# Kernel optimization log

Measured on AMD Instinct MI355X. Metric: run time of the kernel, lower is better.

Reference implementation:

```python
import jax, jax.numpy as jnp
import numpy as np

N = 100_000      # nodes
E = 1_600_000    # edges
F_IN = 256       # num_node_features
H = 128          # hidden_dim
G = 1_000        # graphs in batch


def setup_inputs() -> dict:
    key = jax.random.key(0)
    ks = jax.random.split(key, 12)
    x = jax.random.normal(ks[0], (N, F_IN), jnp.float32)
    edge_index = jax.random.randint(ks[1], (2, E), 0, N)
    batch = jnp.sort(jax.random.randint(ks[2], (N,), 0, G))
    def w(k, shape):
        fan_in = shape[0]
        return jax.random.normal(k, shape, jnp.float32) / np.sqrt(fan_in)
    return {
        "x": x,
        "edge_index": edge_index,
        "batch": batch,
        "W1": w(ks[3], (F_IN, H)), "b1": jnp.zeros((H,), jnp.float32),
        "W2": w(ks[4], (H, H)),    "b2": jnp.zeros((H,), jnp.float32),
        "W3": w(ks[5], (H, H)),    "b3": jnp.zeros((H,), jnp.float32),
        "fw1": w(ks[6], (H, 32)),  "fb1": jnp.zeros((32,), jnp.float32),
        "fw2": w(ks[7], (32, 2)),  "fb2": jnp.zeros((2,), jnp.float32),
    }


def reference(x, edge_index, batch, W1, b1, W2, b2, W3, b3, fw1, fb1, fw2, fb2):
    # GCN normalization with self-loops (PyG GCNConv defaults)
    loop = jnp.arange(N)
    src = jnp.concatenate([edge_index[0], loop])  # [E+N]
    dst = jnp.concatenate([edge_index[1], loop])
    deg = jax.ops.segment_sum(jnp.ones(E + N, x.dtype), dst, num_segments=N)
    dis = jnp.where(deg > 0, jax.lax.rsqrt(deg), 0.0)
    norm = (dis[src] * dis[dst])[:, None]  # [E+N, 1]

    def gcn(h, W, b):
        h = h @ W                                    # linear transform first (fewer bytes moved)
        msg = h[src] * norm                          # gather + scale
        return jax.ops.segment_sum(msg, dst, num_segments=N) + b  # scatter-add

    h = jax.nn.relu(gcn(x, W1, b1))   # dropout = identity (eval mode)
    h = jax.nn.relu(gcn(h, W2, b2))
    h = jax.nn.relu(gcn(h, W3, b3))

    # global_mean_pool over graph ids
    sums = jax.ops.segment_sum(h, batch, num_segments=G)          # [G, H]
    cnt = jax.ops.segment_sum(jnp.ones(N, h.dtype), batch, num_segments=G)
    g = sums / jnp.maximum(cnt, 1.0)[:, None]

    g = jax.nn.relu(g @ fw1 + fb1)
    logits = g @ fw2 + fb2
    return jax.nn.log_softmax(logits, axis=1)
```

## Files before the change

### kernel.cpp

```cpp
#include <hip/hip_runtime.h>
#include <hip/hip_bf16.h>
#include <math.h>

#define N_NODES 100000
#define N_EDGES 1600000
#define F_IN 256
#define H_DIM 128
#define N_GRAPHS 1000

#define NB_BUCKETS ((N_NODES + 255) >> 8)
#define BSTRIDE 392
#define A_BLOCKS 256
#define EPB (N_EDGES / A_BLOCKS)

typedef unsigned short bfu;
typedef unsigned char u8;
typedef short short8 __attribute__((ext_vector_type(8)));
typedef float f32x4 __attribute__((ext_vector_type(4)));
typedef float f32x2 __attribute__((ext_vector_type(2)));

__device__ __forceinline__ float b2f(unsigned u) {
    union { unsigned int i; float f; } v;
    v.i = u << 16;
    return v.f;
}
__device__ __forceinline__ bfu f2b(float f) {
    __hip_bfloat16 h = __float2bfloat16(f);
    return *reinterpret_cast<bfu*>(&h);
}
__device__ __forceinline__ unsigned pk4_fp8(float v0, float v1, float v2, float v3) {
    int r = __builtin_amdgcn_cvt_pk_fp8_f32(v0, v1, 0, false);
    r = __builtin_amdgcn_cvt_pk_fp8_f32(v2, v3, r, true);
    return (unsigned)r;
}
__device__ __forceinline__ void acc4_fp8(float* a, unsigned v) {
    f32x2 p;
    p = __builtin_amdgcn_cvt_pk_f32_fp8((int)v, false); a[0] += p.x; a[1] += p.y;
    p = __builtin_amdgcn_cvt_pk_f32_fp8((int)v, true);  a[2] += p.x; a[3] += p.y;
}
__device__ __forceinline__ void acc16_fp8(float* a, uint4 v) {
    acc4_fp8(a, v.x); acc4_fp8(a + 4, v.y); acc4_fp8(a + 8, v.z); acc4_fp8(a + 12, v.w);
}

__global__ __launch_bounds__(256) void k_hist(const int* __restrict__ dst,
                                              int* __restrict__ cnt_bb) {
    __shared__ int h[BSTRIDE];
    const int t = threadIdx.x;
    for (int i = t; i < BSTRIDE; i += 256) h[i] = 0;
    __syncthreads();
    const int base = blockIdx.x * EPB;
    for (int i = t; i < EPB; i += 256) atomicAdd(&h[dst[base + i] >> 8], 1);
    __syncthreads();
    for (int i = t; i < NB_BUCKETS; i += 256) cnt_bb[blockIdx.x * BSTRIDE + i] = h[i];
}

__global__ __launch_bounds__(256) void k_scan_blocks(int* __restrict__ cnt_bb,
                                                     int* __restrict__ btot) {
    __shared__ int s[256];
    const int t = threadIdx.x;
    const int b = blockIdx.x;
    int v = cnt_bb[t * BSTRIDE + b];
    s[t] = v;
    __syncthreads();
    for (int off = 1; off < 256; off <<= 1) {
        int u = (t >= off) ? s[t - off] : 0;
        __syncthreads();
        s[t] += u;
        __syncthreads();
    }
    cnt_bb[t * BSTRIDE + b] = s[t] - v;
    if (t == 255) btot[b] = s[255];
}

__global__ __launch_bounds__(512) void k_scan_buckets(const int* __restrict__ btot,
                                                      int* __restrict__ bucket_base) {
    __shared__ int s[512];
    const int t = threadIdx.x;
    int v = (t < NB_BUCKETS) ? btot[t] : 0;
    s[t] = v;
    __syncthreads();
    for (int off = 1; off < 512; off <<= 1) {
        int u = (t >= off) ? s[t - off] : 0;
        __syncthreads();
        s[t] += u;
        __syncthreads();
    }
    if (t < NB_BUCKETS) bucket_base[t] = s[t] - v;
    if (t == 0) bucket_base[NB_BUCKETS] = N_EDGES;
}

__global__ __launch_bounds__(256) void k_stage(const int* __restrict__ src,
                                               const int* __restrict__ dst,
                                               const int* __restrict__ cnt_bb,
                                               const int* __restrict__ bucket_base,
                                               unsigned* __restrict__ staging) {
    __shared__ int cur[BSTRIDE];
    const int t = threadIdx.x;
    const int blk = blockIdx.x;
    for (int i = t; i < NB_BUCKETS; i += 256)
        cur[i] = bucket_base[i] + cnt_bb[blk * BSTRIDE + i];
    __syncthreads();
    const int base = blk * EPB;
    for (int i = t; i < EPB; i += 256) {
        int d = dst[base + i];
        int s = src[base + i];
        int b = d >> 8;
        int pos = atomicAdd(&cur[b], 1);
        staging[pos] = (unsigned)s | ((unsigned)(d & 255) << 24);
    }
}

__global__ __launch_bounds__(256) void k_bucket(const unsigned* __restrict__ staging,
                                                const int* __restrict__ bucket_base,
                                                int* __restrict__ row_ptr,
                                                float* __restrict__ dis,
                                                int* __restrict__ col) {
    __shared__ int h[256];
    __shared__ int sc[256];
    __shared__ int cur[256];
    const int t = threadIdx.x;
    const int b = blockIdx.x;
    const int s0 = bucket_base[b];
    const int ne = bucket_base[b + 1] - s0;
    h[t] = 0;
    __syncthreads();
    for (int i = t; i < ne; i += 256) atomicAdd(&h[staging[s0 + i] >> 24], 1);
    __syncthreads();
    int myc = h[t];
    sc[t] = myc;
    __syncthreads();
    for (int off = 1; off < 256; off <<= 1) {
        int u = (t >= off) ? sc[t - off] : 0;
        __syncthreads();
        sc[t] += u;
        __syncthreads();
    }
    int excl = sc[t] - myc;
    int node = b * 256 + t;
    if (node <= N_NODES) row_ptr[node] = s0 + excl;
    if (node < N_NODES) dis[node] = rsqrtf((float)(myc + 1));
    cur[t] = s0 + excl;
    __syncthreads();
    for (int i = t; i < ne; i += 256) {
        unsigned u = staging[s0 + i];
        int pos = atomicAdd(&cur[u >> 24], 1);
        col[pos] = (int)(u & 0xFFFFFFu);
    }
}

__device__ __forceinline__ void wpack_one(const float* __restrict__ W,
                                          bfu* __restrict__ Wp, int u) {
    int lane = u & 63;
    int nf = (u >> 6) & 7;
    int ks = u >> 9;
    int k = ks * 32 + (lane >> 4) * 8;
    int n = nf * 16 + (lane & 15);
    bfu o[8];
#pragma unroll
    for (int j = 0; j < 8; ++j) o[j] = f2b(W[(k + j) * 128 + n]);
    uint4 pk;
    pk.x = (unsigned)o[0] | ((unsigned)o[1] << 16);
    pk.y = (unsigned)o[2] | ((unsigned)o[3] << 16);
    pk.z = (unsigned)o[4] | ((unsigned)o[5] << 16);
    pk.w = (unsigned)o[6] | ((unsigned)o[7] << 16);
    *(uint4*)&Wp[u * 8] = pk;
}

__global__ __launch_bounds__(256) void k_misc(const float* __restrict__ W1,
                                              const float* __restrict__ W2,
                                              const float* __restrict__ W3,
                                              bfu* __restrict__ wp1, bfu* __restrict__ wp2,
                                              bfu* __restrict__ wp3,
                                              const int* __restrict__ batch,
                                              int* __restrict__ bounds) {
    const int b = blockIdx.x, t = threadIdx.x;
    if (b < 16) {
        wpack_one(W1, wp1, b * 256 + t);
    } else if (b < 24) {
        wpack_one(W2, wp2, (b - 16) * 256 + t);
    } else if (b < 32) {
        wpack_one(W3, wp3, (b - 24) * 256 + t);
    } else {
        int g = (b - 32) * 256 + t;
        if (g <= N_GRAPHS) {
            int lo = 0, hi = N_NODES;
            while (lo < hi) {
                int mid = (lo + hi) >> 1;
                if (batch[mid] < g) lo = mid + 1; else hi = mid;
            }
            bounds[g] = lo;
        }
    }
}

__global__ __launch_bounds__(256, 4) void k_mm1(const float* __restrict__ A,
                                                const bfu* __restrict__ Wp,
                                                const float* __restrict__ dis,
                                                u8* __restrict__ C8, int M) {
    const int t = threadIdx.x;
    const int w = t >> 6, l = t & 63, l15 = l & 15, lhi = l >> 4;
    const int row = blockIdx.x * 64 + w * 16 + l15;
    const int rowc = row < M ? row : M - 1;
    const float* ap = A + (long)rowc * 256 + lhi * 8;

    float4 va[8][2];
#pragma unroll
    for (int ks = 0; ks < 8; ++ks) {
        va[ks][0] = *(const float4*)(ap + ks * 32);
        va[ks][1] = *(const float4*)(ap + ks * 32 + 4);
    }

    f32x4 acc[8];
#pragma unroll
    for (int nf = 0; nf < 8; ++nf) acc[nf] = (f32x4)0.0f;

#pragma unroll
    for (int ks = 0; ks < 8; ++ks) {
        unsigned p0 = (unsigned)f2b(va[ks][0].x) | ((unsigned)f2b(va[ks][0].y) << 16);
        unsigned p1 = (unsigned)f2b(va[ks][0].z) | ((unsigned)f2b(va[ks][0].w) << 16);
        unsigned p2 = (unsigned)f2b(va[ks][1].x) | ((unsigned)f2b(va[ks][1].y) << 16);
        unsigned p3 = (unsigned)f2b(va[ks][1].z) | ((unsigned)f2b(va[ks][1].w) << 16);
        uint4 afu = make_uint4(p0, p1, p2, p3);
        short8 af = *(short8*)&afu;
        const bfu* wp = Wp + ((long)(ks * 8) * 64 + l) * 8;
#pragma unroll
        for (int nf = 0; nf < 8; ++nf) {
            short8 wf = *(const short8*)(wp + (long)nf * 64 * 8);
            acc[nf] = __builtin_amdgcn_mfma_f32_16x16x32_bf16(wf, af, acc[nf], 0, 0, 0);
        }
    }
    if (row < M) {
        float sc = dis[row];
        int nb0 = lhi * 4;
#pragma unroll
        for (int nf = 0; nf < 8; ++nf) {
            unsigned pk = pk4_fp8(acc[nf][0] * sc, acc[nf][1] * sc,
                                  acc[nf][2] * sc, acc[nf][3] * sc);
            *(unsigned*)&C8[(long)row * 128 + nf * 16 + nb0] = pk;
        }
    }
}

__global__ __launch_bounds__(256) void k_agg_mm(const int* __restrict__ row_ptr,
                                                const int* __restrict__ col,
                                                const float* __restrict__ dis,
                                                const u8* __restrict__ tprev8,
                                                const float* __restrict__ bvec,
                                                const bfu* __restrict__ Wp,
                                                u8* __restrict__ tnext8, int M) {
    __shared__ bfu Hs[64 * 136];
    const int t = threadIdx.x;
    const int nrow = t >> 2;
    const int node = blockIdx.x * 64 + nrow;
    const int lz = t & 3;
    const int ch = lz * 32;

    if (node < M) {
        float a[32];
#pragma unroll
        for (int j = 0; j < 32; ++j) a[j] = 0.0f;
        const u8* tp = tprev8 + ch;
        {
            const u8* r = tp + (long)node * 128;
            acc16_fp8(a, *(const uint4*)r);
            acc16_fp8(a + 16, *(const uint4*)(r + 16));
        }
        int e = row_ptr[node];
        const int end = row_ptr[node + 1];
        for (; e + 1 < end; e += 2) {
            int s0 = col[e], s1 = col[e + 1];
            const u8* r0 = tp + (long)s0 * 128;
            const u8* r1 = tp + (long)s1 * 128;
            uint4 v00 = *(const uint4*)r0;
            uint4 v01 = *(const uint4*)(r0 + 16);
            uint4 v10 = *(const uint4*)r1;
            uint4 v11 = *(const uint4*)(r1 + 16);
            acc16_fp8(a, v00); acc16_fp8(a + 16, v01);
            acc16_fp8(a, v10); acc16_fp8(a + 16, v11);
        }
        if (e < end) {
            const u8* r = tp + (long)col[e] * 128;
            acc16_fp8(a, *(const uint4*)r);
            acc16_fp8(a + 16, *(const uint4*)(r + 16));
        }
        const float dn = dis[node];
        uint pk[16];
#pragma unroll
        for (int j = 0; j < 16; ++j) {
            float lo = fmaxf(a[2 * j] * dn + bvec[ch + 2 * j], 0.0f);
            float hi = fmaxf(a[2 * j + 1] * dn + bvec[ch + 2 * j + 1], 0.0f);
            pk[j] = (unsigned)f2b(lo) | ((unsigned)f2b(hi) << 16);
        }
        bfu* hrow = &Hs[nrow * 136 + ch];
#pragma unroll
        for (int q = 0; q < 4; ++q)
            *(uint4*)(hrow + q * 8) = make_uint4(pk[4 * q], pk[4 * q + 1], pk[4 * q + 2], pk[4 * q + 3]);
    }
    __syncthreads();
    const int w = t >> 6, l = t & 63, l15 = l & 15, lhi = l >> 4;
    f32x4 acc[8];
#pragma unroll
    for (int nf = 0; nf < 8; ++nf) acc[nf] = (f32x4)0.0f;
#pragma unroll
    for (int ks = 0; ks < 4; ++ks) {
        short8 af = *(const short8*)&Hs[(w * 16 + l15) * 136 + ks * 32 + lhi * 8];
        const bfu* wp = Wp + ((long)(ks * 8) * 64 + l) * 8;
#pragma unroll
        for (int nf = 0; nf < 8; ++nf) {
            short8 wf = *(const short8*)(wp + (long)nf * 64 * 8);
            acc[nf] = __builtin_amdgcn_mfma_f32_16x16x32_bf16(wf, af, acc[nf], 0, 0, 0);
        }
    }
    int row = blockIdx.x * 64 + w * 16 + l15;
    if (row < M) {
        float sc = dis[row];
        int nb0 = lhi * 4;
#pragma unroll
        for (int nf = 0; nf < 8; ++nf) {
            unsigned pko = pk4_fp8(acc[nf][0] * sc, acc[nf][1] * sc,
                                   acc[nf][2] * sc, acc[nf][3] * sc);
            *(unsigned*)&tnext8[(long)row * 128 + nf * 16 + nb0] = pko;
        }
    }
}

__global__ __launch_bounds__(256) void k_agg8(const int* __restrict__ row_ptr,
                                              const int* __restrict__ col,
                                              const float* __restrict__ dis,
                                              const u8* __restrict__ t8,
                                              const float* __restrict__ b,
                                              bfu* __restrict__ h) {
    const int t = threadIdx.x;
    const int node = blockIdx.x * 8 + (t >> 5);
    const int lane = t & 31;
    if (node >= N_NODES) return;
    const int q = lane << 2;

    const u8* tp = t8 + q;
    float a[4] = {0.f, 0.f, 0.f, 0.f};
    acc4_fp8(a, *(const unsigned*)&tp[(long)node * 128]);

    int e = row_ptr[node];
    const int end = row_ptr[node + 1];
    for (; e + 3 < end; e += 4) {
        int s0 = col[e], s1 = col[e + 1], s2 = col[e + 2], s3 = col[e + 3];
        unsigned v0 = *(const unsigned*)&tp[(long)s0 * 128];
        unsigned v1 = *(const unsigned*)&tp[(long)s1 * 128];
        unsigned v2 = *(const unsigned*)&tp[(long)s2 * 128];
        unsigned v3 = *(const unsigned*)&tp[(long)s3 * 128];
        acc4_fp8(a, v0); acc4_fp8(a, v1); acc4_fp8(a, v2); acc4_fp8(a, v3);
    }
    for (; e < end; ++e)
        acc4_fp8(a, *(const unsigned*)&tp[(long)col[e] * 128]);

    const float dn = dis[node];
    float4 bb = *(const float4*)&b[q];
    float o0 = fmaxf(a[0] * dn + bb.x, 0.0f);
    float o1 = fmaxf(a[1] * dn + bb.y, 0.0f);
    float o2 = fmaxf(a[2] * dn + bb.z, 0.0f);
    float o3 = fmaxf(a[3] * dn + bb.w, 0.0f);
    uint2 pk;
    pk.x = (unsigned)f2b(o0) | ((unsigned)f2b(o1) << 16);
    pk.y = (unsigned)f2b(o2) | ((unsigned)f2b(o3) << 16);
    *(uint2*)&h[(long)node * 128 + q] = pk;
}

__global__ __launch_bounds__(128) void k_pool_head(const int* __restrict__ bounds,
                                                   const bfu* __restrict__ h,
                                                   const float* __restrict__ fw1, const float* __restrict__ fb1,
                                                   const float* __restrict__ fw2, const float* __restrict__ fb2,
                                                   float* __restrict__ out) {
    const int g = blockIdx.x;
    const int t = threadIdx.x;
    const int s = bounds[g], e = bounds[g + 1];
    float sum = 0.0f;
    int n = s;
    for (; n + 1 < e; n += 2) {
        sum += b2f(h[(long)n * 128 + t]);
        sum += b2f(h[(long)(n + 1) * 128 + t]);
    }
    if (n < e) sum += b2f(h[(long)n * 128 + t]);

    __shared__ float sg[128];
    __shared__ float sh[32];
    float inv = 1.0f / fmaxf((float)(e - s), 1.0f);
    sg[t] = sum * inv;
    __syncthreads();
    if (t < 32) {
        float a = fb1[t];
#pragma unroll 8
        for (int k = 0; k < 128; ++k) a += sg[k] * fw1[k * 32 + t];
        sh[t] = fmaxf(a, 0.0f);
    }
    __syncthreads();
    if (t == 0) {
        float l0 = fb2[0], l1 = fb2[1];
        for (int k = 0; k < 32; ++k) {
            l0 += sh[k] * fw2[k * 2];
            l1 += sh[k] * fw2[k * 2 + 1];
        }
        float m = fmaxf(l0, l1);
        float lse = m + logf(expf(l0 - m) + expf(l1 - m));
        out[g * 2 + 0] = l0 - lse;
        out[g * 2 + 1] = l1 - lse;
    }
}

extern "C" void kernel_launch(void* const* d_in, const int* in_sizes, int n_in,
                              void* d_out, int out_size, void* d_ws, size_t ws_size,
                              hipStream_t stream) {
    const float* x  = (const float*)d_in[0];
    const int* ei   = (const int*)d_in[1];
    const int* batch = (const int*)d_in[2];
    const float* W1 = (const float*)d_in[3];
    const float* b1 = (const float*)d_in[4];
    const float* W2 = (const float*)d_in[5];
    const float* b2 = (const float*)d_in[6];
    const float* W3 = (const float*)d_in[7];
    const float* b3 = (const float*)d_in[8];
    const float* fw1 = (const float*)d_in[9];
    const float* fb1 = (const float*)d_in[10];
    const float* fw2 = (const float*)d_in[11];
    const float* fb2 = (const float*)d_in[12];
    float* out = (float*)d_out;

    const int* src = ei;
    const int* dst = ei + N_EDGES;

    char* ws = (char*)d_ws;
    int*      cnt_bb      = (int*)ws;
    int*      btot        = cnt_bb + A_BLOCKS * BSTRIDE;
    int*      bucket_base = btot + BSTRIDE;
    unsigned* staging     = (unsigned*)(bucket_base + BSTRIDE + 8);
    int*      row_ptr     = (int*)(staging + N_EDGES);
    float*    dis         = (float*)(row_ptr + N_NODES + 4);
    int*      col         = (int*)(dis + N_NODES);
    int*      bounds      = col + N_EDGES;
    bfu*      wpack1      = (bfu*)(bounds + N_GRAPHS + 8);
    bfu*      wpack2      = wpack1 + 32768;
    bfu*      wpack3      = wpack2 + 16384;
    u8*       bufA8       = (u8*)(wpack3 + 16384);
    u8*       bufB8       = bufA8 + (long)N_NODES * 128;
    u8*       bufC8       = bufB8 + (long)N_NODES * 128;
    bfu*      bufD        = (bfu*)(bufC8 + (long)N_NODES * 128);

    k_hist<<<A_BLOCKS, 256, 0, stream>>>(dst, cnt_bb);
    k_scan_blocks<<<NB_BUCKETS, 256, 0, stream>>>(cnt_bb, btot);
    k_scan_buckets<<<1, 512, 0, stream>>>(btot, bucket_base);
    k_stage<<<A_BLOCKS, 256, 0, stream>>>(src, dst, cnt_bb, bucket_base, staging);
    k_bucket<<<NB_BUCKETS, 256, 0, stream>>>(staging, bucket_base, row_ptr, dis, col);
    k_misc<<<36, 256, 0, stream>>>(W1, W2, W3, wpack1, wpack2, wpack3, batch, bounds);

    const int mm1Grid = (N_NODES + 63) / 64;
    const int fusedGrid = (N_NODES + 63) / 64;
    const int aggGrid = (N_NODES + 7) / 8;

    k_mm1<<<mm1Grid, 256, 0, stream>>>(x, wpack1, dis, bufA8, N_NODES);
    k_agg_mm<<<fusedGrid, 256, 0, stream>>>(row_ptr, col, dis, bufA8, b1, wpack2, bufB8, N_NODES);
    k_agg_mm<<<fusedGrid, 256, 0, stream>>>(row_ptr, col, dis, bufB8, b2, wpack3, bufC8, N_NODES);
    k_agg8<<<aggGrid, 256, 0, stream>>>(row_ptr, col, dis, bufC8, b3, bufD);

    k_pool_head<<<N_GRAPHS, 128, 0, stream>>>(bounds, bufD, fw1, fb1, fw2, fb2, out);
}
```

Baseline: 310.2 us.

## Unfuse aggregation and matmul into separate agg8 and mm2 kernels

```diff
diff --git a/kernel.cpp b/kernel.cpp
--- a/kernel.cpp
+++ b/kernel.cpp
@@ -37,9 +37,6 @@
     f32x2 p;
     p = __builtin_amdgcn_cvt_pk_f32_fp8((int)v, false); a[0] += p.x; a[1] += p.y;
     p = __builtin_amdgcn_cvt_pk_f32_fp8((int)v, true);  a[2] += p.x; a[3] += p.y;
-}
-__device__ __forceinline__ void acc16_fp8(float* a, uint4 v) {
-    acc4_fp8(a, v.x); acc4_fp8(a + 4, v.y); acc4_fp8(a + 8, v.z); acc4_fp8(a + 12, v.w);
 }
 
 __global__ __launch_bounds__(256) void k_hist(const int* __restrict__ dst,
@@ -241,89 +238,6 @@
     }
 }
 
-__global__ __launch_bounds__(256) void k_agg_mm(const int* __restrict__ row_ptr,
-                                                const int* __restrict__ col,
-                                                const float* __restrict__ dis,
-                                                const u8* __restrict__ tprev8,
-                                                const float* __restrict__ bvec,
-                                                const bfu* __restrict__ Wp,
-                                                u8* __restrict__ tnext8, int M) {
-    __shared__ bfu Hs[64 * 136];
-    const int t = threadIdx.x;
-    const int nrow = t >> 2;
-    const int node = blockIdx.x * 64 + nrow;
-    const int lz = t & 3;
-    const int ch = lz * 32;
-
-    if (node < M) {
-        float a[32];
-#pragma unroll
-        for (int j = 0; j < 32; ++j) a[j] = 0.0f;
-        const u8* tp = tprev8 + ch;
-        {
-            const u8* r = tp + (long)node * 128;
-            acc16_fp8(a, *(const uint4*)r);
-            acc16_fp8(a + 16, *(const uint4*)(r + 16));
-        }
-        int e = row_ptr[node];
-        const int end = row_ptr[node + 1];
-        for (; e + 1 < end; e += 2) {
-            int s0 = col[e], s1 = col[e + 1];
-            const u8* r0 = tp + (long)s0 * 128;
-            const u8* r1 = tp + (long)s1 * 128;
-            uint4 v00 = *(const uint4*)r0;
-            uint4 v01 = *(const uint4*)(r0 + 16);
-            uint4 v10 = *(const uint4*)r1;
-            uint4 v11 = *(const uint4*)(r1 + 16);
-            acc16_fp8(a, v00); acc16_fp8(a + 16, v01);
-            acc16_fp8(a, v10); acc16_fp8(a + 16, v11);
-        }
-        if (e < end) {
-            const u8* r = tp + (long)col[e] * 128;
-            acc16_fp8(a, *(const uint4*)r);
-            acc16_fp8(a + 16, *(const uint4*)(r + 16));
-        }
-        const float dn = dis[node];
-        uint pk[16];
-#pragma unroll
-        for (int j = 0; j < 16; ++j) {
-            float lo = fmaxf(a[2 * j] * dn + bvec[ch + 2 * j], 0.0f);
-            float hi = fmaxf(a[2 * j + 1] * dn + bvec[ch + 2 * j + 1], 0.0f);
-            pk[j] = (unsigned)f2b(lo) | ((unsigned)f2b(hi) << 16);
-        }
-        bfu* hrow = &Hs[nrow * 136 + ch];
-#pragma unroll
-        for (int q = 0; q < 4; ++q)
-            *(uint4*)(hrow + q * 8) = make_uint4(pk[4 * q], pk[4 * q + 1], pk[4 * q + 2], pk[4 * q + 3]);
-    }
-    __syncthreads();
-    const int w = t >> 6, l = t & 63, l15 = l & 15, lhi = l >> 4;
-    f32x4 acc[8];
-#pragma unroll
-    for (int nf = 0; nf < 8; ++nf) acc[nf] = (f32x4)0.0f;
-#pragma unroll
-    for (int ks = 0; ks < 4; ++ks) {
-        short8 af = *(const short8*)&Hs[(w * 16 + l15) * 136 + ks * 32 + lhi * 8];
-        const bfu* wp = Wp + ((long)(ks * 8) * 64 + l) * 8;
-#pragma unroll
-        for (int nf = 0; nf < 8; ++nf) {
-            short8 wf = *(const short8*)(wp + (long)nf * 64 * 8);
-            acc[nf] = __builtin_amdgcn_mfma_f32_16x16x32_bf16(wf, af, acc[nf], 0, 0, 0);
-        }
-    }
-    int row = blockIdx.x * 64 + w * 16 + l15;
-    if (row < M) {
-        float sc = dis[row];
-        int nb0 = lhi * 4;
-#pragma unroll
-        for (int nf = 0; nf < 8; ++nf) {
-            unsigned pko = pk4_fp8(acc[nf][0] * sc, acc[nf][1] * sc,
-                                   acc[nf][2] * sc, acc[nf][3] * sc);
-            *(unsigned*)&tnext8[(long)row * 128 + nf * 16 + nb0] = pko;
-        }
-    }
-}
-
 __global__ __launch_bounds__(256) void k_agg8(const int* __restrict__ row_ptr,
                                               const int* __restrict__ col,
                                               const float* __restrict__ dis,
@@ -342,12 +256,18 @@
 
     int e = row_ptr[node];
     const int end = row_ptr[node + 1];
+    for (; e + 7 < end; e += 8) {
+        unsigned v[8];
+#pragma unroll
+        for (int j = 0; j < 8; ++j) v[j] = *(const unsigned*)&tp[(long)col[e + j] * 128];
+#pragma unroll
+        for (int j = 0; j < 8; ++j) acc4_fp8(a, v[j]);
+    }
     for (; e + 3 < end; e += 4) {
-        int s0 = col[e], s1 = col[e + 1], s2 = col[e + 2], s3 = col[e + 3];
-        unsigned v0 = *(const unsigned*)&tp[(long)s0 * 128];
-        unsigned v1 = *(const unsigned*)&tp[(long)s1 * 128];
-        unsigned v2 = *(const unsigned*)&tp[(long)s2 * 128];
-        unsigned v3 = *(const unsigned*)&tp[(long)s3 * 128];
+        unsigned v0 = *(const unsigned*)&tp[(long)col[e] * 128];
+        unsigned v1 = *(const unsigned*)&tp[(long)col[e + 1] * 128];
+        unsigned v2 = *(const unsigned*)&tp[(long)col[e + 2] * 128];
+        unsigned v3 = *(const unsigned*)&tp[(long)col[e + 3] * 128];
         acc4_fp8(a, v0); acc4_fp8(a, v1); acc4_fp8(a, v2); acc4_fp8(a, v3);
     }
     for (; e < end; ++e)
@@ -363,6 +283,62 @@
     pk.x = (unsigned)f2b(o0) | ((unsigned)f2b(o1) << 16);
     pk.y = (unsigned)f2b(o2) | ((unsigned)f2b(o3) << 16);
     *(uint2*)&h[(long)node * 128 + q] = pk;
+}
+
+__global__ __launch_bounds__(256) void k_mm2(const bfu* __restrict__ A,
+                                             const bfu* __restrict__ Wp,
+                                             const float* __restrict__ dis,
+                                             u8* __restrict__ C8, int M) {
+    __shared__ bfu As[2][64 * 40];
+    const int t = threadIdx.x;
+    const int w = t >> 6;
+    const int l = t & 63;
+    const int l15 = l & 15;
+    const int lhi = l >> 4;
+    const int row0 = blockIdx.x * 64;
+
+    f32x4 acc[8];
+#pragma unroll
+    for (int nf = 0; nf < 8; ++nf) acc[nf] = (f32x4)0.0f;
+
+    uint4 pb = make_uint4(0u, 0u, 0u, 0u);
+    {
+        int r = t >> 2, s = t & 3;
+        if (row0 + r < M) pb = *(const uint4*)&A[(long)(row0 + r) * 128 + s * 8];
+    }
+
+    int buf = 0;
+#pragma unroll
+    for (int ks = 0; ks < 4; ++ks) {
+        *(uint4*)&As[buf][(t >> 2) * 40 + (t & 3) * 8] = pb;
+        if (ks + 1 < 4) {
+            const int k0n = (ks + 1) * 32;
+            int r = t >> 2, s = t & 3;
+            pb = make_uint4(0u, 0u, 0u, 0u);
+            if (row0 + r < M) pb = *(const uint4*)&A[(long)(row0 + r) * 128 + k0n + s * 8];
+        }
+        __syncthreads();
+        short8 af = *(const short8*)&As[buf][(w * 16 + l15) * 40 + lhi * 8];
+        const bfu* wp = Wp + ((long)(ks * 8) * 64 + l) * 8;
+#pragma unroll
+        for (int nf = 0; nf < 8; ++nf) {
+            short8 wf = *(const short8*)(wp + (long)nf * 64 * 8);
+            acc[nf] = __builtin_amdgcn_mfma_f32_16x16x32_bf16(wf, af, acc[nf], 0, 0, 0);
+        }
+        if (ks + 1 < 4) __syncthreads();
+        buf ^= 1;
+    }
+    int row = row0 + w * 16 + l15;
+    if (row < M) {
+        float sc = dis[row];
+        int nb0 = lhi * 4;
+#pragma unroll
+        for (int nf = 0; nf < 8; ++nf) {
+            unsigned pko = pk4_fp8(acc[nf][0] * sc, acc[nf][1] * sc,
+                                   acc[nf][2] * sc, acc[nf][3] * sc);
+            *(unsigned*)&C8[(long)row * 128 + nf * 16 + nb0] = pko;
+        }
+    }
 }
 
 __global__ __launch_bounds__(128) void k_pool_head(const int* __restrict__ bounds,
@@ -439,10 +415,8 @@
     bfu*      wpack1      = (bfu*)(bounds + N_GRAPHS + 8);
     bfu*      wpack2      = wpack1 + 32768;
     bfu*      wpack3      = wpack2 + 16384;
-    u8*       bufA8       = (u8*)(wpack3 + 16384);
-    u8*       bufB8       = bufA8 + (long)N_NODES * 128;
-    u8*       bufC8       = bufB8 + (long)N_NODES * 128;
-    bfu*      bufD        = (bfu*)(bufC8 + (long)N_NODES * 128);
+    u8*       bufT8       = (u8*)(wpack3 + 16384);
+    bfu*      bufH        = (bfu*)(bufT8 + (long)N_NODES * 128);
 
     k_hist<<<A_BLOCKS, 256, 0, stream>>>(dst, cnt_bb);
     k_scan_blocks<<<NB_BUCKETS, 256, 0, stream>>>(cnt_bb, btot);
@@ -452,13 +426,15 @@
     k_misc<<<36, 256, 0, stream>>>(W1, W2, W3, wpack1, wpack2, wpack3, batch, bounds);
 
     const int mm1Grid = (N_NODES + 63) / 64;
-    const int fusedGrid = (N_NODES + 63) / 64;
+    const int mm2Grid = (N_NODES + 63) / 64;
     const int aggGrid = (N_NODES + 7) / 8;
 
-    k_mm1<<<mm1Grid, 256, 0, stream>>>(x, wpack1, dis, bufA8, N_NODES);
-    k_agg_mm<<<fusedGrid, 256, 0, stream>>>(row_ptr, col, dis, bufA8, b1, wpack2, bufB8, N_NODES);
-    k_agg_mm<<<fusedGrid, 256, 0, stream>>>(row_ptr, col, dis, bufB8, b2, wpack3, bufC8, N_NODES);
-    k_agg8<<<aggGrid, 256, 0, stream>>>(row_ptr, col, dis, bufC8, b3, bufD);
-
-    k_pool_head<<<N_GRAPHS, 128, 0, stream>>>(bounds, bufD, fw1, fb1, fw2, fb2, out);
-}
+    k_mm1<<<mm1Grid, 256, 0, stream>>>(x, wpack1, dis, bufT8, N_NODES);
+    k_agg8<<<aggGrid, 256, 0, stream>>>(row_ptr, col, dis, bufT8, b1, bufH);
+    k_mm2<<<mm2Grid, 256, 0, stream>>>(bufH, wpack2, dis, bufT8, N_NODES);
+    k_agg8<<<aggGrid, 256, 0, stream>>>(row_ptr, col, dis, bufT8, b2, bufH);
+    k_mm2<<<mm2Grid, 256, 0, stream>>>(bufH, wpack3, dis, bufT8, N_NODES);
+    k_agg8<<<aggGrid, 256, 0, stream>>>(row_ptr, col, dis, bufT8, b3, bufH);
+
+    k_pool_head<<<N_GRAPHS, 128, 0, stream>>>(bounds, bufH, fw1, fb1, fw2, fb2, out);
+}
```

Result: no change. 305.3 us (-1.6%).
